# Kernel optimization log

Hardware: AMD Instinct MI355X
Metric: run time of the kernel (lower is better)

The kernel has to match this reference:

```python
import jax, jax.numpy as jnp
import numpy as np
import math

NH, KS, KR, VS, HID, RS = 8, 32, 8, 32, 256, 16
TOTAL = 2 * KS + VS + KR  # 104


def setup_inputs() -> dict:
    key = jax.random.key(0)
    ks = jax.random.split(key, 10)
    B, S = 4, 512
    H = jax.random.normal(ks[0], (B, S, HID), dtype=jnp.float32)
    route_data = jax.random.normal(ks[1], (B, S, S, RS), dtype=jnp.float32)
    attention_mask = jnp.zeros((B, 1, 1, S), dtype=jnp.float32)
    W_qkv = jax.random.normal(ks[2], (NH * TOTAL, HID), dtype=jnp.float32) * 0.02
    Wd = jax.random.normal(ks[3], (NH * KR, RS), dtype=jnp.float32) * 0.02
    Wroute = jax.random.normal(ks[4], (NH * VS, RS), dtype=jnp.float32) * 0.02
    W_out = jax.random.normal(ks[5], (HID, NH * VS), dtype=jnp.float32) * 0.02
    b_out = jnp.zeros((HID,), dtype=jnp.float32)
    ln_w = jnp.ones((HID,), dtype=jnp.float32)
    ln_b = jnp.zeros((HID,), dtype=jnp.float32)
    return {"H": H, "route_data": route_data, "attention_mask": attention_mask,
            "W_qkv": W_qkv, "Wd": Wd, "Wroute": Wroute,
            "W_out": W_out, "b_out": b_out, "ln_w": ln_w, "ln_b": ln_b}


def reference(H, route_data, attention_mask, W_qkv, Wd, Wroute, W_out, b_out, ln_w, ln_b):
    B, S, _ = H.shape
    # fused QKVQr projection: [B,S,NH,TOTAL] -> [B,NH,S,TOTAL]
    H2 = (H @ W_qkv.T).reshape(B, S, NH, TOTAL).transpose(0, 2, 1, 3)
    Qn = H2[..., :KS]
    Kn = H2[..., KS:2 * KS]
    V = H2[..., 2 * KS:2 * KS + VS]
    Qr = H2[..., 2 * KS + VS:]
    # route keys: [B,i,j,NH,KR]
    Kr = (route_data @ Wd.T).reshape(B, S, S, NH, KR)
    QKr = jnp.einsum('bhik,bijhk->bhij', Qr, Kr)
    scale = 1.0 / math.sqrt(KS + KR)
    scores = scale * (jnp.einsum('bhik,bhjk->bhij', Qn, Kn) + QKr) + attention_mask
    probs = jax.nn.softmax(scores, axis=-1)
    ctx = jnp.einsum('bhij,bhjv->bhiv', probs, V)
    # route values: [B,i,j,NH,VS]
    Vr = (route_data @ Wroute.T).reshape(B, S, S, NH, VS)
    ctx = ctx + jnp.einsum('bhij,bijhv->bhiv', probs, Vr)
    ctx = ctx.transpose(0, 2, 1, 3).reshape(B, S, NH * VS)
    # output projection + TF-style LayerNorm, residual added AFTER norm
    out = ctx @ W_out.T + b_out
    u = out.mean(-1, keepdims=True)
    s = ((out - u) ** 2).mean(-1, keepdims=True)
    ln = ln_w * (out - u) / jnp.sqrt(s + 1e-12) + ln_b
    return ln + H
```

## Files before the change

### kernel.cpp

```cpp
#include <hip/hip_runtime.h>
#include <cmath>

#define B_    4
#define S_    512
#define NH_   8
#define TOT_  104
#define NQKV_ 832
#define ROWS_ 2048

typedef float f32x4 __attribute__((ext_vector_type(4)));
typedef short short8 __attribute__((ext_vector_type(8)));

__device__ inline float bfu2f(unsigned int bits16) {
  union { unsigned int i; float f; } v; v.i = bits16 << 16; return v.f;
}
__device__ inline unsigned short f2bf(float f) {
  union { float f; unsigned int i; } v; v.f = f;
  unsigned int r = v.i + 0x7fffu + ((v.i >> 16) & 1u);
  return (unsigned short)(r >> 16);
}
__device__ inline short8 ld8(const unsigned short* p) {
  union { uint4 u; short8 s; } v; v.u = *(const uint4*)p; return v.s;
}

__global__ __launch_bounds__(256) void castf2bf(const float* __restrict__ in,
                                                unsigned short* __restrict__ outp) {
  int idx = blockIdx.x * 256 + threadIdx.x;
  float4 v = ((const float4*)in)[idx];
  uint2 u;
  u.x = (unsigned int)f2bf(v.x) | ((unsigned int)f2bf(v.y) << 16);
  u.y = (unsigned int)f2bf(v.z) | ((unsigned int)f2bf(v.w) << 16);
  ((uint2*)outp)[idx] = u;
}

__global__ __launch_bounds__(256) void k1_qkv(const unsigned short* __restrict__ Hbf,
                                              const unsigned short* __restrict__ Wqb,
                                              unsigned short* __restrict__ Qnb,
                                              unsigned short* __restrict__ Knb,
                                              unsigned short* __restrict__ Vtb,
                                              float* __restrict__ Qr) {
  const int t = threadIdx.x;
  const int w = t >> 6, l = t & 63;
  const int lm = l & 15, lk = (l >> 4) << 3;
  const int i0 = blockIdx.y * 64 + w * 16;
  const int n0 = blockIdx.x * 64;
  f32x4 acc[4] = {};
  for (int k0 = 0; k0 < 256; k0 += 32) {
    short8 a = ld8(Hbf + (size_t)(i0 + lm) * 256 + k0 + lk);
#pragma unroll
    for (int nf = 0; nf < 4; ++nf) {
      short8 b = ld8(Wqb + (size_t)(n0 + nf * 16 + lm) * 256 + k0 + lk);
      acc[nf] = __builtin_amdgcn_mfma_f32_16x16x32_bf16(a, b, acc[nf], 0, 0, 0);
    }
  }
  const int rbase = i0 + ((l >> 4) << 2);
#pragma unroll
  for (int nf = 0; nf < 4; ++nf) {
#pragma unroll
    for (int r = 0; r < 4; ++r) {
      int row = rbase + r;
      int c = n0 + nf * 16 + lm;
      int b_ = row >> 9, i = row & 511;
      int h = c / 104, o = c - h * 104;
      float v = acc[nf][r];
      size_t bh = (size_t)(b_ * 8 + h);
      if (o < 32)       Qnb[(bh * 512 + i) * 32 + o] = f2bf(v);
      else if (o < 64)  Knb[(bh * 512 + i) * 32 + (o - 32)] = f2bf(v);
      else if (o < 96)  Vtb[(bh * 32 + (o - 64)) * 512 + i] = f2bf(v);
      else              Qr[(size_t)row * 64 + h * 8 + (o - 96)] = v;
    }
  }
}

__global__ __launch_bounds__(256) void k1c_qrr(const float* __restrict__ Qr,
                                               const float* __restrict__ Wd,
                                               float* __restrict__ qrrg) {
  int t = threadIdx.x;
  int row = blockIdx.x * 2 + (t >> 7);
  int c = t & 127, h = c >> 4, r = c & 15;
  float s = 0.f;
#pragma unroll
  for (int k = 0; k < 8; ++k)
    s += Qr[(size_t)row * 64 + h * 8 + k] * Wd[(h * 8 + k) * 16 + r];
  qrrg[(size_t)row * 128 + c] = s;
}

__global__ __launch_bounds__(256) void k2_qk(const unsigned short* __restrict__ Qnb,
                                             const unsigned short* __restrict__ Knb,
                                             unsigned short* __restrict__ sqk) {
  const int t = threadIdx.x;
  const int w = t >> 6, l = t & 63;
  const int lm = l & 15, lk = (l >> 4) << 3;
  const int bh = blockIdx.z;
  const int i0 = blockIdx.y * 64 + w * 16, j0 = blockIdx.x * 64;
  short8 a = ld8(Qnb + ((size_t)bh * 512 + i0 + lm) * 32 + lk);
  f32x4 acc[4] = {};
#pragma unroll
  for (int nf = 0; nf < 4; ++nf) {
    short8 b = ld8(Knb + ((size_t)bh * 512 + j0 + nf * 16 + lm) * 32 + lk);
    acc[nf] = __builtin_amdgcn_mfma_f32_16x16x32_bf16(a, b, acc[nf], 0, 0, 0);
  }
  const int rbase = i0 + ((l >> 4) << 2);
#pragma unroll
  for (int nf = 0; nf < 4; ++nf)
#pragma unroll
    for (int r = 0; r < 4; ++r)
      sqk[((size_t)bh * 512 + rbase + r) * 512 + j0 + nf * 16 + lm] = f2bf(acc[nf][r]);
}

__global__ __launch_bounds__(256) void k3_route(const float* __restrict__ rd,
                                                const unsigned short* __restrict__ sqk,
                                                const float* __restrict__ qrrg,
                                                const float* __restrict__ Wroute,
                                                const float* __restrict__ mask,
                                                unsigned short* __restrict__ probs,
                                                float* __restrict__ ctx) {
  __shared__ float rdf[512][17];
  __shared__ unsigned int sc_bf[8][257];
  __shared__ float qrr[8][16];
  __shared__ float prp[4][64][2];
  __shared__ float prf[8][16];
  const int t = threadIdx.x;
  const int row = blockIdx.x, b = row >> 9, i = row & 511;

  const float4* rp = (const float4*)(rd + (size_t)row * 8192);
#pragma unroll
  for (int q = 0; q < 8; ++q) {
    int idx = q * 256 + t;
    float4 v = rp[idx];
    int j = idx >> 2, c0 = (idx & 3) * 4;
    rdf[j][c0] = v.x; rdf[j][c0 + 1] = v.y; rdf[j][c0 + 2] = v.z; rdf[j][c0 + 3] = v.w;
  }
  if (t < 128) ((float*)qrr)[t] = qrrg[(size_t)row * 128 + t];
  __syncthreads();

  const float scal = 0.15811388300841898f;
  {
    float rlo[16], rhi[16];
#pragma unroll
    for (int q = 0; q < 4; ++q) {
      float4 a = *(const float4*)&rdf[t][q * 4];
      float4 c = *(const float4*)&rdf[t + 256][q * 4];
      rlo[q*4]=a.x; rlo[q*4+1]=a.y; rlo[q*4+2]=a.z; rlo[q*4+3]=a.w;
      rhi[q*4]=c.x; rhi[q*4+1]=c.y; rhi[q*4+2]=c.z; rhi[q*4+3]=c.w;
    }
    float mlo = mask[b * 512 + t], mhi = mask[b * 512 + t + 256];
#pragma unroll
    for (int h = 0; h < 8; ++h) {
      float slo = 0.f, shi = 0.f;
#pragma unroll
      for (int r = 0; r < 16; ++r) { slo += qrr[h][r] * rlo[r]; shi += qrr[h][r] * rhi[r]; }
      const unsigned short* qp = sqk + ((size_t)(b * 8 + h) * 512 + i) * 512;
      float qlo = bfu2f(qp[t]), qhi = bfu2f(qp[t + 256]);
      float vlo = scal * (qlo + slo) + mlo;
      float vhi = scal * (qhi + shi) + mhi;
      sc_bf[h][t] = (unsigned int)f2bf(vlo) | ((unsigned int)f2bf(vhi) << 16);
    }
  }
  __syncthreads();

  const int wave = t >> 6, lane = t & 63;
  for (int hh = 0; hh < 2; ++hh) {
    int h = wave * 2 + hh;
    float vlo[4], vhi[4];
    float m = -1e30f;
#pragma unroll
    for (int cq = 0; cq < 4; ++cq) {
      unsigned int u = sc_bf[h][lane + 64 * cq];
      vlo[cq] = bfu2f(u & 0xffffu); vhi[cq] = bfu2f(u >> 16);
      m = fmaxf(m, fmaxf(vlo[cq], vhi[cq]));
    }
#pragma unroll
    for (int o = 32; o; o >>= 1) m = fmaxf(m, __shfl_xor(m, o));
    float ssum = 0.f;
#pragma unroll
    for (int cq = 0; cq < 4; ++cq) {
      vlo[cq] = __expf(vlo[cq] - m); vhi[cq] = __expf(vhi[cq] - m);
      ssum += vlo[cq] + vhi[cq];
    }
#pragma unroll
    for (int o = 32; o; o >>= 1) ssum += __shfl_xor(ssum, o);
    float inv = 1.0f / ssum;
    unsigned short* pout = probs + ((size_t)(b * 8 + h) * 512 + i) * 512;
#pragma unroll
    for (int cq = 0; cq < 4; ++cq) {
      int jj = lane + 64 * cq;
      unsigned short plo = f2bf(vlo[cq] * inv), phi = f2bf(vhi[cq] * inv);
      pout[jj] = plo; pout[jj + 256] = phi;
      sc_bf[h][jj] = (unsigned int)plo | ((unsigned int)phi << 16);
    }
  }
  __syncthreads();

  {
    int c = t & 63, qj = t >> 6;
    int h = c >> 3, ru = c & 7;
    float p0 = 0.f, p1 = 0.f;
    for (int jj = qj * 64; jj < qj * 64 + 64; ++jj) {
      unsigned int u = sc_bf[h][jj];
      float plo = bfu2f(u & 0xffffu), phi = bfu2f(u >> 16);
      p0 += plo * rdf[jj][2 * ru]     + phi * rdf[jj + 256][2 * ru];
      p1 += plo * rdf[jj][2 * ru + 1] + phi * rdf[jj + 256][2 * ru + 1];
    }
    prp[qj][c][0] = p0; prp[qj][c][1] = p1;
  }
  __syncthreads();
  if (t < 128) {
    int h = t >> 4, r = t & 15;
    int c = h * 8 + (r >> 1), part = r & 1;
    prf[h][r] = prp[0][c][part] + prp[1][c][part] + prp[2][c][part] + prp[3][c][part];
  }
  __syncthreads();

  {
    int h = t >> 5;
    float s = 0.f;
#pragma unroll
    for (int r = 0; r < 16; ++r) s += prf[h][r] * Wroute[t * 16 + r];
    ctx[(size_t)row * 256 + t] = s;
  }
}

__global__ __launch_bounds__(256) void k4_pv(const unsigned short* __restrict__ probs,
                                             const unsigned short* __restrict__ Vtb,
                                             float* __restrict__ ctx) {
  const int t = threadIdx.x;
  const int w = t >> 6, l = t & 63;
  const int lm = l & 15, lk = (l >> 4) << 3;
  const int bh = blockIdx.y;
  const int b = bh >> 3, h = bh & 7;
  const int irow = blockIdx.x * 64 + w * 16 + lm;
  f32x4 acc[2] = {};
  for (int k0 = 0; k0 < 512; k0 += 32) {
    short8 a = ld8(probs + ((size_t)bh * 512 + irow) * 512 + k0 + lk);
#pragma unroll
    for (int nf = 0; nf < 2; ++nf) {
      short8 bb = ld8(Vtb + ((size_t)bh * 32 + nf * 16 + lm) * 512 + k0 + lk);
      acc[nf] = __builtin_amdgcn_mfma_f32_16x16x32_bf16(a, bb, acc[nf], 0, 0, 0);
    }
  }
  const int rbase = blockIdx.x * 64 + w * 16 + ((l >> 4) << 2);
#pragma unroll
  for (int nf = 0; nf < 2; ++nf)
#pragma unroll
    for (int r = 0; r < 4; ++r) {
      size_t addr = ((size_t)b * 512 + rbase + r) * 256 + h * 32 + nf * 16 + lm;
      ctx[addr] += acc[nf][r];
    }
}

__global__ __launch_bounds__(256) void k5_out(const float* __restrict__ ctx,
                                              const float* __restrict__ Wout,
                                              const float* __restrict__ bout,
                                              const float* __restrict__ lnw,
                                              const float* __restrict__ lnb,
                                              const float* __restrict__ Hin,
                                              float* __restrict__ out) {
  __shared__ float buf[8][257];
  __shared__ float uarr[8], rarr[8];
  const int t = threadIdx.x;
  const int R0 = blockIdx.x * 8;
  {
    int sr = t >> 5, c0 = (t & 31) * 8;
    const float4* cp = (const float4*)(ctx + (size_t)(R0 + sr) * 256 + c0);
    float4 a = cp[0], bq = cp[1];
    buf[sr][c0+0]=a.x;  buf[sr][c0+1]=a.y;  buf[sr][c0+2]=a.z;  buf[sr][c0+3]=a.w;
    buf[sr][c0+4]=bq.x; buf[sr][c0+5]=bq.y; buf[sr][c0+6]=bq.z; buf[sr][c0+7]=bq.w;
  }
  __syncthreads();

  float o[8];
  {
    float bo = bout[t];
#pragma unroll
    for (int r = 0; r < 8; ++r) o[r] = bo;
  }
  const float4* wp = (const float4*)(Wout + (size_t)t * 256);
  for (int d4 = 0; d4 < 64; ++d4) {
    float4 w = wp[d4];
    int d = d4 * 4;
#pragma unroll
    for (int r = 0; r < 8; ++r)
      o[r] += buf[r][d]*w.x + buf[r][d+1]*w.y + buf[r][d+2]*w.z + buf[r][d+3]*w.w;
  }
  __syncthreads();
#pragma unroll
  for (int r = 0; r < 8; ++r) buf[r][t] = o[r];
  __syncthreads();
  {
    int wave = t >> 6, lane = t & 63;
#pragma unroll
    for (int rr = 0; rr < 2; ++rr) {
      int r = wave * 2 + rr;
      float s = 0.f, sq = 0.f;
#pragma unroll
      for (int c = 0; c < 4; ++c) {
        float x = buf[r][lane + 64*c];
        s += x; sq += x*x;
      }
#pragma unroll
      for (int off = 32; off; off >>= 1) {
        s += __shfl_xor(s, off);
        sq += __shfl_xor(sq, off);
      }
      if (lane == 0) {
        float u = s * (1.0f/256.0f);
        uarr[r] = u;
        rarr[r] = rsqrtf(sq * (1.0f/256.0f) - u*u + 1e-12f);
      }
    }
  }
  __syncthreads();
  {
    float lw = lnw[t], lb = lnb[t];
#pragma unroll
    for (int r = 0; r < 8; ++r) {
      size_t R = R0 + r;
      out[R * 256 + t] = lw * (o[r] - uarr[r]) * rarr[r] + lb + Hin[R * 256 + t];
    }
  }
}

extern "C" void kernel_launch(void* const* d_in, const int* in_sizes, int n_in,
                              void* d_out, int out_size, void* d_ws, size_t ws_size,
                              hipStream_t stream) {
  const float* Hin    = (const float*)d_in[0];
  const float* rd     = (const float*)d_in[1];
  const float* mask   = (const float*)d_in[2];
  const float* Wqkv   = (const float*)d_in[3];
  const float* Wd     = (const float*)d_in[4];
  const float* Wroute = (const float*)d_in[5];
  const float* Wout   = (const float*)d_in[6];
  const float* bout   = (const float*)d_in[7];
  const float* lnw    = (const float*)d_in[8];
  const float* lnb    = (const float*)d_in[9];
  float* out = (float*)d_out;

  unsigned short* Hbf   = (unsigned short*)d_ws;
  unsigned short* Wqb   = Hbf + 524288;
  unsigned short* Qnb   = Wqb + 212992;
  unsigned short* Knb   = Qnb + 524288;
  unsigned short* Vtb   = Knb + 524288;
  unsigned short* sqk   = Vtb + 524288;
  unsigned short* probs = sqk + 8388608;
  float* Qr   = (float*)(probs + 8388608);
  float* qrrg = Qr + 131072;
  float* ctx  = qrrg + 262144;

  castf2bf<<<512,            256, 0, stream>>>(Hin, Hbf);
  castf2bf<<<208,            256, 0, stream>>>(Wqkv, Wqb);
  k1_qkv  <<<dim3(13, 32),   256, 0, stream>>>(Hbf, Wqb, Qnb, Knb, Vtb, Qr);
  k1c_qrr <<<1024,           256, 0, stream>>>(Qr, Wd, qrrg);
  k2_qk   <<<dim3(8, 8, 32), 256, 0, stream>>>(Qnb, Knb, sqk);
  k3_route<<<2048,           256, 0, stream>>>(rd, sqk, qrrg, Wroute, mask, probs, ctx);
  k4_pv   <<<dim3(8, 32),    256, 0, stream>>>(probs, Vtb, ctx);
  k5_out  <<<256,            256, 0, stream>>>(ctx, Wout, bout, lnw, lnb, Hin, out);
}
```

Measured before the change: 196.4 us.

## Fuse bf16 casts into QKV GEMM, pack route data as bf16, split PV over K

Drops the two standalone cast kernels so the QKV GEMM reads fp32 H and W_qkv directly and converts them to bf16 in registers. The route kernel now keeps route_data in shared memory as packed bf16 pairs instead of padded fp32, which roughly halves its LDS footprint and may allow higher occupancy, at some cost in precision. The PV kernel is split four ways along the key dimension and accumulates into ctx with atomicAdd, giving more blocks in exchange for atomic traffic and nondeterministic summation order. The output/LayerNorm kernel handles 4 rows per block instead of 8 and launches twice as many blocks.

```diff
diff --git a/kernel.cpp b/kernel.cpp
--- a/kernel.cpp
+++ b/kernel.cpp
@@ -22,19 +22,15 @@
 __device__ inline short8 ld8(const unsigned short* p) {
   union { uint4 u; short8 s; } v; v.u = *(const uint4*)p; return v.s;
 }
-
-__global__ __launch_bounds__(256) void castf2bf(const float* __restrict__ in,
-                                                unsigned short* __restrict__ outp) {
-  int idx = blockIdx.x * 256 + threadIdx.x;
-  float4 v = ((const float4*)in)[idx];
-  uint2 u;
-  u.x = (unsigned int)f2bf(v.x) | ((unsigned int)f2bf(v.y) << 16);
-  u.y = (unsigned int)f2bf(v.z) | ((unsigned int)f2bf(v.w) << 16);
-  ((uint2*)outp)[idx] = u;
-}
-
-__global__ __launch_bounds__(256) void k1_qkv(const unsigned short* __restrict__ Hbf,
-                                              const unsigned short* __restrict__ Wqb,
+__device__ inline short8 pk8(float4 a, float4 b) {
+  union { unsigned short us[8]; short8 s; } v;
+  v.us[0]=f2bf(a.x); v.us[1]=f2bf(a.y); v.us[2]=f2bf(a.z); v.us[3]=f2bf(a.w);
+  v.us[4]=f2bf(b.x); v.us[5]=f2bf(b.y); v.us[6]=f2bf(b.z); v.us[7]=f2bf(b.w);
+  return v.s;
+}
+
+__global__ __launch_bounds__(256) void k1_qkv(const float* __restrict__ Hin,
+                                              const float* __restrict__ Wqkv,
                                               unsigned short* __restrict__ Qnb,
                                               unsigned short* __restrict__ Knb,
                                               unsigned short* __restrict__ Vtb,
@@ -46,10 +42,12 @@
   const int n0 = blockIdx.x * 64;
   f32x4 acc[4] = {};
   for (int k0 = 0; k0 < 256; k0 += 32) {
-    short8 a = ld8(Hbf + (size_t)(i0 + lm) * 256 + k0 + lk);
+    const float* ap = Hin + (size_t)(i0 + lm) * 256 + k0 + lk;
+    short8 a = pk8(*(const float4*)ap, *(const float4*)(ap + 4));
 #pragma unroll
     for (int nf = 0; nf < 4; ++nf) {
-      short8 b = ld8(Wqb + (size_t)(n0 + nf * 16 + lm) * 256 + k0 + lk);
+      const float* bp = Wqkv + (size_t)(n0 + nf * 16 + lm) * 256 + k0 + lk;
+      short8 b = pk8(*(const float4*)bp, *(const float4*)(bp + 4));
       acc[nf] = __builtin_amdgcn_mfma_f32_16x16x32_bf16(a, b, acc[nf], 0, 0, 0);
     }
   }
@@ -115,7 +113,7 @@
                                                 const float* __restrict__ mask,
                                                 unsigned short* __restrict__ probs,
                                                 float* __restrict__ ctx) {
-  __shared__ float rdf[512][17];
+  __shared__ unsigned int rdp[512][10];
   __shared__ unsigned int sc_bf[8][257];
   __shared__ float qrr[8][16];
   __shared__ float prp[4][64][2];
@@ -128,8 +126,9 @@
   for (int q = 0; q < 8; ++q) {
     int idx = q * 256 + t;
     float4 v = rp[idx];
-    int j = idx >> 2, c0 = (idx & 3) * 4;
-    rdf[j][c0] = v.x; rdf[j][c0 + 1] = v.y; rdf[j][c0 + 2] = v.z; rdf[j][c0 + 3] = v.w;
+    int j = idx >> 2, u0 = (idx & 3) * 2;
+    rdp[j][u0]     = (unsigned int)f2bf(v.x) | ((unsigned int)f2bf(v.y) << 16);
+    rdp[j][u0 + 1] = (unsigned int)f2bf(v.z) | ((unsigned int)f2bf(v.w) << 16);
   }
   if (t < 128) ((float*)qrr)[t] = qrrg[(size_t)row * 128 + t];
   __syncthreads();
@@ -139,10 +138,12 @@
     float rlo[16], rhi[16];
 #pragma unroll
     for (int q = 0; q < 4; ++q) {
-      float4 a = *(const float4*)&rdf[t][q * 4];
-      float4 c = *(const float4*)&rdf[t + 256][q * 4];
-      rlo[q*4]=a.x; rlo[q*4+1]=a.y; rlo[q*4+2]=a.z; rlo[q*4+3]=a.w;
-      rhi[q*4]=c.x; rhi[q*4+1]=c.y; rhi[q*4+2]=c.z; rhi[q*4+3]=c.w;
+      uint2 ua = *(const uint2*)&rdp[t][q * 2];
+      uint2 uc = *(const uint2*)&rdp[t + 256][q * 2];
+      rlo[q*4]   = bfu2f(ua.x & 0xffffu); rlo[q*4+1] = bfu2f(ua.x >> 16);
+      rlo[q*4+2] = bfu2f(ua.y & 0xffffu); rlo[q*4+3] = bfu2f(ua.y >> 16);
+      rhi[q*4]   = bfu2f(uc.x & 0xffffu); rhi[q*4+1] = bfu2f(uc.x >> 16);
+      rhi[q*4+2] = bfu2f(uc.y & 0xffffu); rhi[q*4+3] = bfu2f(uc.y >> 16);
     }
     float mlo = mask[b * 512 + t], mhi = mask[b * 512 + t + 256];
 #pragma unroll
@@ -198,9 +199,11 @@
     float p0 = 0.f, p1 = 0.f;
     for (int jj = qj * 64; jj < qj * 64 + 64; ++jj) {
       unsigned int u = sc_bf[h][jj];
+      unsigned int rr = rdp[jj][ru];
+      unsigned int r2 = rdp[jj + 256][ru];
       float plo = bfu2f(u & 0xffffu), phi = bfu2f(u >> 16);
-      p0 += plo * rdf[jj][2 * ru]     + phi * rdf[jj + 256][2 * ru];
-      p1 += plo * rdf[jj][2 * ru + 1] + phi * rdf[jj + 256][2 * ru + 1];
+      p0 += plo * bfu2f(rr & 0xffffu) + phi * bfu2f(r2 & 0xffffu);
+      p1 += plo * bfu2f(rr >> 16)     + phi * bfu2f(r2 >> 16);
     }
     prp[qj][c][0] = p0; prp[qj][c][1] = p1;
   }
@@ -230,8 +233,9 @@
   const int bh = blockIdx.y;
   const int b = bh >> 3, h = bh & 7;
   const int irow = blockIdx.x * 64 + w * 16 + lm;
+  const int kbase = blockIdx.z * 128;
   f32x4 acc[2] = {};
-  for (int k0 = 0; k0 < 512; k0 += 32) {
+  for (int k0 = kbase; k0 < kbase + 128; k0 += 32) {
     short8 a = ld8(probs + ((size_t)bh * 512 + irow) * 512 + k0 + lk);
 #pragma unroll
     for (int nf = 0; nf < 2; ++nf) {
@@ -245,7 +249,7 @@
 #pragma unroll
     for (int r = 0; r < 4; ++r) {
       size_t addr = ((size_t)b * 512 + rbase + r) * 256 + h * 32 + nf * 16 + lm;
-      ctx[addr] += acc[nf][r];
+      atomicAdd(&ctx[addr], acc[nf][r]);
     }
 }
 
@@ -256,65 +260,60 @@
                                               const float* __restrict__ lnb,
                                               const float* __restrict__ Hin,
                                               float* __restrict__ out) {
-  __shared__ float buf[8][257];
-  __shared__ float uarr[8], rarr[8];
-  const int t = threadIdx.x;
-  const int R0 = blockIdx.x * 8;
-  {
-    int sr = t >> 5, c0 = (t & 31) * 8;
-    const float4* cp = (const float4*)(ctx + (size_t)(R0 + sr) * 256 + c0);
-    float4 a = cp[0], bq = cp[1];
-    buf[sr][c0+0]=a.x;  buf[sr][c0+1]=a.y;  buf[sr][c0+2]=a.z;  buf[sr][c0+3]=a.w;
-    buf[sr][c0+4]=bq.x; buf[sr][c0+5]=bq.y; buf[sr][c0+6]=bq.z; buf[sr][c0+7]=bq.w;
-  }
-  __syncthreads();
-
-  float o[8];
+  __shared__ float buf[4][257];
+  __shared__ float uarr[4], rarr[4];
+  const int t = threadIdx.x;
+  const int R0 = blockIdx.x * 4;
+  {
+    int sr = t >> 6, c0 = (t & 63) * 4;
+    float4 a = *(const float4*)(ctx + (size_t)(R0 + sr) * 256 + c0);
+    buf[sr][c0+0]=a.x; buf[sr][c0+1]=a.y; buf[sr][c0+2]=a.z; buf[sr][c0+3]=a.w;
+  }
+  __syncthreads();
+
+  float o[4];
   {
     float bo = bout[t];
 #pragma unroll
-    for (int r = 0; r < 8; ++r) o[r] = bo;
+    for (int r = 0; r < 4; ++r) o[r] = bo;
   }
   const float4* wp = (const float4*)(Wout + (size_t)t * 256);
   for (int d4 = 0; d4 < 64; ++d4) {
     float4 w = wp[d4];
     int d = d4 * 4;
 #pragma unroll
-    for (int r = 0; r < 8; ++r)
+    for (int r = 0; r < 4; ++r)
       o[r] += buf[r][d]*w.x + buf[r][d+1]*w.y + buf[r][d+2]*w.z + buf[r][d+3]*w.w;
   }
   __syncthreads();
 #pragma unroll
-  for (int r = 0; r < 8; ++r) buf[r][t] = o[r];
+  for (int r = 0; r < 4; ++r) buf[r][t] = o[r];
   __syncthreads();
   {
     int wave = t >> 6, lane = t & 63;
-#pragma unroll
-    for (int rr = 0; rr < 2; ++rr) {
-      int r = wave * 2 + rr;
-      float s = 0.f, sq = 0.f;
-#pragma unroll
-      for (int c = 0; c < 4; ++c) {
-        float x = buf[r][lane + 64*c];
-        s += x; sq += x*x;
-      }
-#pragma unroll
-      for (int off = 32; off; off >>= 1) {
-        s += __shfl_xor(s, off);
-        sq += __shfl_xor(sq, off);
-      }
-      if (lane == 0) {
-        float u = s * (1.0f/256.0f);
-        uarr[r] = u;
-        rarr[r] = rsqrtf(sq * (1.0f/256.0f) - u*u + 1e-12f);
-      }
+    int r = wave;
+    float s = 0.f, sq = 0.f;
+#pragma unroll
+    for (int c = 0; c < 4; ++c) {
+      float x = buf[r][lane + 64*c];
+      s += x; sq += x*x;
+    }
+#pragma unroll
+    for (int off = 32; off; off >>= 1) {
+      s += __shfl_xor(s, off);
+      sq += __shfl_xor(sq, off);
+    }
+    if (lane == 0) {
+      float u = s * (1.0f/256.0f);
+      uarr[r] = u;
+      rarr[r] = rsqrtf(sq * (1.0f/256.0f) - u*u + 1e-12f);
     }
   }
   __syncthreads();
   {
     float lw = lnw[t], lb = lnb[t];
 #pragma unroll
-    for (int r = 0; r < 8; ++r) {
+    for (int r = 0; r < 4; ++r) {
       size_t R = R0 + r;
       out[R * 256 + t] = lw * (o[r] - uarr[r]) * rarr[r] + lb + Hin[R * 256 + t];
     }
@@ -336,9 +335,7 @@
   const float* lnb    = (const float*)d_in[9];
   float* out = (float*)d_out;
 
-  unsigned short* Hbf   = (unsigned short*)d_ws;
-  unsigned short* Wqb   = Hbf + 524288;
-  unsigned short* Qnb   = Wqb + 212992;
+  unsigned short* Qnb   = (unsigned short*)d_ws;
   unsigned short* Knb   = Qnb + 524288;
   unsigned short* Vtb   = Knb + 524288;
   unsigned short* sqk   = Vtb + 524288;
@@ -347,12 +344,10 @@
   float* qrrg = Qr + 131072;
   float* ctx  = qrrg + 262144;
 
-  castf2bf<<<512,            256, 0, stream>>>(Hin, Hbf);
-  castf2bf<<<208,            256, 0, stream>>>(Wqkv, Wqb);
-  k1_qkv  <<<dim3(13, 32),   256, 0, stream>>>(Hbf, Wqb, Qnb, Knb, Vtb, Qr);
-  k1c_qrr <<<1024,           256, 0, stream>>>(Qr, Wd, qrrg);
-  k2_qk   <<<dim3(8, 8, 32), 256, 0, stream>>>(Qnb, Knb, sqk);
-  k3_route<<<2048,           256, 0, stream>>>(rd, sqk, qrrg, Wroute, mask, probs, ctx);
-  k4_pv   <<<dim3(8, 32),    256, 0, stream>>>(probs, Vtb, ctx);
-  k5_out  <<<256,            256, 0, stream>>>(ctx, Wout, bout, lnw, lnb, Hin, out);
-}
+  k1_qkv  <<<dim3(13, 32),      256, 0, stream>>>(Hin, Wqkv, Qnb, Knb, Vtb, Qr);
+  k1c_qrr <<<1024,              256, 0, stream>>>(Qr, Wd, qrrg);
+  k2_qk   <<<dim3(8, 8, 32),    256, 0, stream>>>(Qnb, Knb, sqk);
+  k3_route<<<2048,              256, 0, stream>>>(rd, sqk, qrrg, Wroute, mask, probs, ctx);
+  k4_pv   <<<dim3(8, 32, 4),    256, 0, stream>>>(probs, Vtb, ctx);
+  k5_out  <<<512,               256, 0, stream>>>(ctx, Wout, bout, lnw, lnb, Hin, out);
+}
```

Measured after the change: 196.8 us. Within noise of the previous version (+0.2%).
